# Optimization experiments

Measured on AMD Instinct MI355X. Metric: run time of the kernel, lower is better.

## Reference

```python
import jax, jax.numpy as jnp
import numpy as np

N = 50000   # nodes
C = 128     # channels
H = 2       # heads
E = 800000  # edges (before self loops)


def setup_inputs() -> dict:
    key = jax.random.key(0)
    ks = jax.random.split(key, 8)
    scale = 1.0 / np.sqrt(C)
    x = jax.random.normal(ks[0], (N, C), jnp.float32)
    edge_index = jax.random.randint(ks[1], (2, E), 0, N, jnp.int32)
    W_l = jax.random.normal(ks[2], (H * C, C), jnp.float32) * scale  # lin_l (source/message)
    b_l = jnp.zeros((H * C,), jnp.float32)
    W_r = jax.random.normal(ks[3], (H * C, C), jnp.float32) * scale  # lin_r (target)
    b_r = jnp.zeros((H * C,), jnp.float32)
    att = jax.random.normal(ks[4], (H, C), jnp.float32) * scale      # attention vector per head
    bias = jnp.zeros((C,), jnp.float32)                              # conv output bias (concat=False)
    gn_weight = jnp.ones((C,), jnp.float32)
    gn_bias = jnp.zeros((C,), jnp.float32)
    gn_mean_scale = jnp.ones((C,), jnp.float32)
    return {"x": x, "edge_index": edge_index, "W_l": W_l, "b_l": b_l,
            "W_r": W_r, "b_r": b_r, "att": att, "bias": bias,
            "gn_weight": gn_weight, "gn_bias": gn_bias, "gn_mean_scale": gn_mean_scale}


def reference(x, edge_index, W_l, b_l, W_r, b_r, att, bias, gn_weight, gn_bias, gn_mean_scale):
    n = x.shape[0]
    h, c = att.shape
    # add self loops (PyG default)
    loops = jnp.arange(n, dtype=edge_index.dtype)
    ei = jnp.concatenate([edge_index, jnp.stack([loops, loops])], axis=1)
    src, dst = ei[0], ei[1]
    # GATv2: e_ij = att . leaky_relu(lin_l(x_j) + lin_r(x_i))
    x_l = (x @ W_l.T + b_l).reshape(n, h, c)  # source / message features
    x_r = (x @ W_r.T + b_r).reshape(n, h, c)  # target features
    e = jax.nn.leaky_relu(x_l[src] + x_r[dst], negative_slope=0.2)  # [E', H, C]
    logits = jnp.einsum('ehc,hc->eh', e, att)                        # [E', H]
    # segment softmax over incoming edges of each destination node
    m = jax.ops.segment_max(logits, dst, num_segments=n)             # every node has a self loop
    p = jnp.exp(logits - m[dst])
    s = jax.ops.segment_sum(p, dst, num_segments=n)
    alpha = p / s[dst]                                               # [E', H]
    # weighted scatter-add of messages, then mean over heads (concat=False) + bias
    out = jax.ops.segment_sum(alpha[:, :, None] * x_l[src], dst, num_segments=n)  # [N, H, C]
    out = out.mean(axis=1) + bias                                    # [N, C]
    # GraphNorm (single graph): weight*(x - mean_scale*mean)/sqrt(var+eps) + bias
    mu = out.mean(axis=0)
    o = out - gn_mean_scale * mu
    var = (o * o).mean(axis=0)
    o = gn_weight * o * jax.lax.rsqrt(var + 1e-5) + gn_bias
    o = jax.nn.elu(o)
    return o + x  # residual (shapes match); dropout is identity at eval
```

## Files before the change

kernel.cpp:

```cpp
#include <hip/hip_runtime.h>
#include <stdint.h>

typedef __attribute__((ext_vector_type(8))) short bf16x8;
typedef __attribute__((ext_vector_type(4))) float f32x4;

__device__ inline float u2f(unsigned v){ union{unsigned u; float f;} c; c.u=v; return c.f; }
__device__ inline float f2u_(float){ return 0; }
__device__ inline unsigned short f2bf(float f){
  union{float f; unsigned u;} c; c.f=f;
  unsigned r = c.u + 0x7FFFu + ((c.u>>16)&1u);
  return (unsigned short)(r>>16);
}
__device__ inline unsigned cvtpk_bf16(float lo, float hi){
  unsigned r;
  asm("v_cvt_pk_bf16_f32 %0, %1, %2" : "=v"(r) : "v"(lo), "v"(hi));
  return r;
}
__device__ inline void up8(uint4 u, float4& a0, float4& a1){
  a0.x = u2f(u.x<<16); a0.y = u2f(u.x & 0xFFFF0000u);
  a0.z = u2f(u.y<<16); a0.w = u2f(u.y & 0xFFFF0000u);
  a1.x = u2f(u.z<<16); a1.y = u2f(u.z & 0xFFFF0000u);
  a1.z = u2f(u.w<<16); a1.w = u2f(u.w & 0xFFFF0000u);
}

__global__ void prep_w(const float* __restrict__ Wl, const float* __restrict__ Wr,
                       const float* __restrict__ bl, const float* __restrict__ br,
                       unsigned short* __restrict__ Wb, float* __restrict__ bcat){
  int idx = blockIdx.x*blockDim.x + threadIdx.x;
  if (idx < 512*128){
    int j = idx >> 7, k = idx & 127;
    float v = (j < 256) ? Wl[j*128 + k] : Wr[(j-256)*128 + k];
    Wb[idx] = f2bf(v);
  }
  if (idx < 512) bcat[idx] = (idx < 256) ? bl[idx] : br[idx-256];
}

__launch_bounds__(256)
__global__ void gemm_mfma(const float* __restrict__ x, const unsigned short* __restrict__ Wb,
                          const float* __restrict__ bcat,
                          unsigned short* __restrict__ xl, unsigned short* __restrict__ xr,
                          int n, int* __restrict__ counts, int* __restrict__ total,
                          float* __restrict__ colsum, float* __restrict__ colsq){
  int gid = blockIdx.x*256 + threadIdx.x;
  if (gid < n) counts[gid] = 0;
  if (gid == 0) *total = 0;
  if (gid < 128){ colsum[gid] = 0.f; colsq[gid] = 0.f; }

  int wave = threadIdx.x >> 6, lane = threadIdx.x & 63;
  int lr = lane & 15, kb = (lane >> 4) * 8;
  int rowbase = blockIdx.x*128 + wave*32;

  union FR { bf16x8 v; unsigned u[4]; uint4 u4; };
  FR bfr[2][4];
  int myrow[2]; bool wr[2];
  #pragma unroll
  for (int rg = 0; rg < 2; ++rg){
    myrow[rg] = rowbase + rg*16 + lr;
    int rc = myrow[rg] < n ? myrow[rg] : n-1;
    wr[rg] = myrow[rg] < n;
    const float* xp = &x[(size_t)rc*128];
    #pragma unroll
    for (int ks = 0; ks < 4; ++ks){
      float4 f0 = *reinterpret_cast<const float4*>(xp + ks*32 + kb);
      float4 f1 = *reinterpret_cast<const float4*>(xp + ks*32 + kb + 4);
      bfr[rg][ks].u[0] = cvtpk_bf16(f0.x, f0.y);
      bfr[rg][ks].u[1] = cvtpk_bf16(f0.z, f0.w);
      bfr[rg][ks].u[2] = cvtpk_bf16(f1.x, f1.y);
      bfr[rg][ks].u[3] = cvtpk_bf16(f1.z, f1.w);
    }
  }

  #pragma unroll 1
  for (int mt = 0; mt < 32; ++mt){
    FR afr[4];
    const unsigned short* wp = &Wb[(size_t)(mt*16 + lr)*128 + kb];
    #pragma unroll
    for (int ks = 0; ks < 4; ++ks)
      afr[ks].u4 = *reinterpret_cast<const uint4*>(wp + ks*32);
    f32x4 acc0 = (f32x4){0.f,0.f,0.f,0.f};
    f32x4 acc1 = (f32x4){0.f,0.f,0.f,0.f};
    #pragma unroll
    for (int ks = 0; ks < 4; ++ks){
      acc0 = __builtin_amdgcn_mfma_f32_16x16x32_bf16(afr[ks].v, bfr[0][ks].v, acc0, 0,0,0);
      acc1 = __builtin_amdgcn_mfma_f32_16x16x32_bf16(afr[ks].v, bfr[1][ks].v, acc1, 0,0,0);
    }
    int ch0 = mt*16 + (lane>>4)*4;
    float4 bi = *reinterpret_cast<const float4*>(&bcat[ch0]);
    unsigned short* dst = (ch0 < 256) ? xl : xr;
    int cc = ch0 & 255;
    if (wr[0]){
      uint2 o; o.x = cvtpk_bf16(acc0[0]+bi.x, acc0[1]+bi.y);
      o.y = cvtpk_bf16(acc0[2]+bi.z, acc0[3]+bi.w);
      *reinterpret_cast<uint2*>(&dst[(size_t)myrow[0]*256 + cc]) = o;
    }
    if (wr[1]){
      uint2 o; o.x = cvtpk_bf16(acc1[0]+bi.x, acc1[1]+bi.y);
      o.y = cvtpk_bf16(acc1[2]+bi.z, acc1[3]+bi.w);
      *reinterpret_cast<uint2*>(&dst[(size_t)myrow[1]*256 + cc]) = o;
    }
  }
}

__global__ void hist_dst(const int* __restrict__ ei, int E, int* __restrict__ counts,
                         int* __restrict__ rank){
  for (int e = blockIdx.x*blockDim.x + threadIdx.x; e < E; e += gridDim.x*blockDim.x)
    rank[e] = atomicAdd(&counts[ei[E + e]], 1);
}

__global__ void alloc_offsets(const int* __restrict__ counts, int n, int* __restrict__ offs,
                              int* __restrict__ total){
  int i = blockIdx.x*blockDim.x + threadIdx.x;
  int lane = threadIdx.x & 63;
  int v = (i < n) ? counts[i] : 0;
  int incl = v;
  #pragma unroll
  for (int d = 1; d < 64; d <<= 1){
    int y = __shfl_up(incl, d);
    if (lane >= d) incl += y;
  }
  int wsum = __shfl(incl, 63);
  int base = 0;
  if (lane == 0) base = atomicAdd(total, wsum);
  base = __shfl(base, 0);
  if (i < n) offs[i] = base + incl - v;
}

__global__ void scatter_edges(const int* __restrict__ ei, int E,
                              const int* __restrict__ offs, const int* __restrict__ rank,
                              int* __restrict__ ssrc){
  for (int e = blockIdx.x*blockDim.x + threadIdx.x; e < E; e += gridDim.x*blockDim.x){
    int d = ei[E + e];
    ssrc[offs[d] + rank[e]] = ei[e];
  }
}

__device__ inline float dot8(const float4& a0, const float4& a1,
                             const float4& xr0, const float4& xr1,
                             const float4& at0, const float4& at1){
  float t, d;
  t = a0.x+xr0.x; t = fmaxf(t, 0.2f*t); d  = at0.x*t;
  t = a0.y+xr0.y; t = fmaxf(t, 0.2f*t); d += at0.y*t;
  t = a0.z+xr0.z; t = fmaxf(t, 0.2f*t); d += at0.z*t;
  t = a0.w+xr0.w; t = fmaxf(t, 0.2f*t); d += at0.w*t;
  t = a1.x+xr1.x; t = fmaxf(t, 0.2f*t); d += at1.x*t;
  t = a1.y+xr1.y; t = fmaxf(t, 0.2f*t); d += at1.y*t;
  t = a1.z+xr1.z; t = fmaxf(t, 0.2f*t); d += at1.z*t;
  t = a1.w+xr1.w; t = fmaxf(t, 0.2f*t); d += at1.w*t;
  return d;
}
__device__ inline float red16(float d){
  d += __shfl_xor(d, 1); d += __shfl_xor(d, 2);
  d += __shfl_xor(d, 4); d += __shfl_xor(d, 8);
  return d;
}

__launch_bounds__(128)
__global__ void node_attn(const unsigned short* __restrict__ xl,
                          const unsigned short* __restrict__ xr,
                          const float* __restrict__ att, const float* __restrict__ bias,
                          const int* __restrict__ offs, const int* __restrict__ counts,
                          const int* __restrict__ ssrc,
                          float* __restrict__ out, int n){
  int lane = threadIdx.x & 63;
  int v = blockIdx.x*2 + (threadIdx.x >> 6);
  if (v >= n) return;
  int half = lane >> 5, q5 = lane & 31, h = q5 >> 4, cq = q5 & 15;
  int fbase = h*128 + cq*8;

  float4 xr0, xr1;
  up8(*reinterpret_cast<const uint4*>(&xr[(size_t)v*256 + fbase]), xr0, xr1);
  float4 at0 = *reinterpret_cast<const float4*>(&att[fbase]);
  float4 at1 = *reinterpret_cast<const float4*>(&att[fbase + 4]);

  float4 sv0, sv1;
  up8(*reinterpret_cast<const uint4*>(&xl[(size_t)v*256 + fbase]), sv0, sv1);
  float dself = red16(dot8(sv0, sv1, xr0, xr1, at0, at1));
  float m, s; float4 ac0, ac1;
  if (half == 0){ m = dself; s = 1.f; ac0 = sv0; ac1 = sv1; }
  else { m = -1e30f; s = 0.f; ac0 = make_float4(0,0,0,0); ac1 = ac0; }

  int e0 = offs[v], cnt = counts[v];
  int halfoff = half*4;
  int e = 0;
  while (e < cnt){
    int take = cnt - e; if (take > 64) take = 64;
    int last = e0 + cnt - 1;
    int idx = e0 + e + lane; if (idx > last) idx = last;
    int batch = ssrc[idx];

    uint4 c0, c1, c2, c3;
    {
      int b = halfoff;
      int i0 = __shfl(batch, b),   i1 = __shfl(batch, b+1);
      int i2 = __shfl(batch, b+2), i3 = __shfl(batch, b+3);
      c0 = *reinterpret_cast<const uint4*>(&xl[(size_t)i0*256 + fbase]);
      c1 = *reinterpret_cast<const uint4*>(&xl[(size_t)i1*256 + fbase]);
      c2 = *reinterpret_cast<const uint4*>(&xl[(size_t)i2*256 + fbase]);
      c3 = *reinterpret_cast<const uint4*>(&xl[(size_t)i3*256 + fbase]);
    }
    for (int j = 0; j < take; j += 8){
      uint4 n0, n1, n2, n3;
      bool more = (j + 8) < take;
      if (more){
        int b = j + 8 + halfoff;
        int i0 = __shfl(batch, b),   i1 = __shfl(batch, b+1);
        int i2 = __shfl(batch, b+2), i3 = __shfl(batch, b+3);
        n0 = *reinterpret_cast<const uint4*>(&xl[(size_t)i0*256 + fbase]);
        n1 = *reinterpret_cast<const uint4*>(&xl[(size_t)i1*256 + fbase]);
        n2 = *reinterpret_cast<const uint4*>(&xl[(size_t)i2*256 + fbase]);
        n3 = *reinterpret_cast<const uint4*>(&xl[(size_t)i3*256 + fbase]);
      }
      float4 a00,a01,a10,a11,a20,a21,a30,a31;
      up8(c0, a00, a01); up8(c1, a10, a11);
      up8(c2, a20, a21); up8(c3, a30, a31);
      float d0 = red16(dot8(a00,a01,xr0,xr1,at0,at1));
      float d1 = red16(dot8(a10,a11,xr0,xr1,at0,at1));
      float d2 = red16(dot8(a20,a21,xr0,xr1,at0,at1));
      float d3 = red16(dot8(a30,a31,xr0,xr1,at0,at1));

      float p0e, p1e, p2e, p3e, f;
      if (j + 8 <= take){
        float nm = fmaxf(m, fmaxf(fmaxf(d0,d1), fmaxf(d2,d3)));
        f = __expf(m - nm);
        p0e = __expf(d0-nm); p1e = __expf(d1-nm);
        p2e = __expf(d2-nm); p3e = __expf(d3-nm);
        m = nm;
      } else {
        int b0 = j + halfoff;
        bool v0 = b0 < take, v1 = b0+1 < take, v2 = b0+2 < take, v3 = b0+3 < take;
        float dm0 = v0 ? d0 : -1e30f, dm1 = v1 ? d1 : -1e30f;
        float dm2 = v2 ? d2 : -1e30f, dm3 = v3 ? d3 : -1e30f;
        float nm = fmaxf(m, fmaxf(fmaxf(dm0,dm1), fmaxf(dm2,dm3)));
        f = __expf(m - nm);
        p0e = v0 ? __expf(d0-nm) : 0.f;
        p1e = v1 ? __expf(d1-nm) : 0.f;
        p2e = v2 ? __expf(d2-nm) : 0.f;
        p3e = v3 ? __expf(d3-nm) : 0.f;
        m = nm;
      }
      s = s*f + ((p0e+p1e)+(p2e+p3e));
      ac0.x = ac0.x*f + p0e*a00.x + p1e*a10.x + p2e*a20.x + p3e*a30.x;
      ac0.y = ac0.y*f + p0e*a00.y + p1e*a10.y + p2e*a20.y + p3e*a30.y;
      ac0.z = ac0.z*f + p0e*a00.z + p1e*a10.z + p2e*a20.z + p3e*a30.z;
      ac0.w = ac0.w*f + p0e*a00.w + p1e*a10.w + p2e*a20.w + p3e*a30.w;
      ac1.x = ac1.x*f + p0e*a01.x + p1e*a11.x + p2e*a21.x + p3e*a31.x;
      ac1.y = ac1.y*f + p0e*a01.y + p1e*a11.y + p2e*a21.y + p3e*a31.y;
      ac1.z = ac1.z*f + p0e*a01.z + p1e*a11.z + p2e*a21.z + p3e*a31.z;
      ac1.w = ac1.w*f + p0e*a01.w + p1e*a11.w + p2e*a21.w + p3e*a31.w;
      if (more){ c0 = n0; c1 = n1; c2 = n2; c3 = n3; }
    }
    e += take;
  }

  float mo = __shfl_xor(m, 32), so = __shfl_xor(s, 32);
  float4 bo0, bo1;
  bo0.x = __shfl_xor(ac0.x, 32); bo0.y = __shfl_xor(ac0.y, 32);
  bo0.z = __shfl_xor(ac0.z, 32); bo0.w = __shfl_xor(ac0.w, 32);
  bo1.x = __shfl_xor(ac1.x, 32); bo1.y = __shfl_xor(ac1.y, 32);
  bo1.z = __shfl_xor(ac1.z, 32); bo1.w = __shfl_xor(ac1.w, 32);
  float mm = fmaxf(m, mo);
  float fa = __expf(m - mm), fb = __expf(mo - mm);
  s = s*fa + so*fb;
  ac0.x = ac0.x*fa + bo0.x*fb; ac0.y = ac0.y*fa + bo0.y*fb;
  ac0.z = ac0.z*fa + bo0.z*fb; ac0.w = ac0.w*fa + bo0.w*fb;
  ac1.x = ac1.x*fa + bo1.x*fb; ac1.y = ac1.y*fa + bo1.y*fb;
  ac1.z = ac1.z*fa + bo1.z*fb; ac1.w = ac1.w*fa + bo1.w*fb;
  float inv = 1.f/s;
  float w0x = ac0.x*inv, w0y = ac0.y*inv, w0z = ac0.z*inv, w0w = ac0.w*inv;
  float w1x = ac1.x*inv, w1y = ac1.y*inv, w1z = ac1.z*inv, w1w = ac1.w*inv;
  float o0x = __shfl_xor(w0x, 16), o0y = __shfl_xor(w0y, 16);
  float o0z = __shfl_xor(w0z, 16), o0w = __shfl_xor(w0w, 16);
  float o1x = __shfl_xor(w1x, 16), o1y = __shfl_xor(w1y, 16);
  float o1z = __shfl_xor(w1z, 16), o1w = __shfl_xor(w1w, 16);
  if (half == 0 && h == 0){
    float4 b0 = *reinterpret_cast<const float4*>(&bias[cq*8]);
    float4 b1 = *reinterpret_cast<const float4*>(&bias[cq*8 + 4]);
    float4 r0, r1;
    r0.x = 0.5f*(w0x+o0x) + b0.x; r0.y = 0.5f*(w0y+o0y) + b0.y;
    r0.z = 0.5f*(w0z+o0z) + b0.z; r0.w = 0.5f*(w0w+o0w) + b0.w;
    r1.x = 0.5f*(w1x+o1x) + b1.x; r1.y = 0.5f*(w1y+o1y) + b1.y;
    r1.z = 0.5f*(w1z+o1z) + b1.z; r1.w = 0.5f*(w1w+o1w) + b1.w;
    *reinterpret_cast<float4*>(&out[(size_t)v*128 + cq*8])     = r0;
    *reinterpret_cast<float4*>(&out[(size_t)v*128 + cq*8 + 4]) = r1;
  }
}

__global__ void col_reduce(const float* __restrict__ out, int n,
                           float* __restrict__ colsum, float* __restrict__ colsq){
  __shared__ float s1[256*4], s2[256*4];
  int t = threadIdx.x;
  int c4 = t & 31, rg = t >> 5;
  float4 sum = make_float4(0,0,0,0), sq = make_float4(0,0,0,0);
  for (int r = blockIdx.x*8 + rg; r < n; r += gridDim.x*8){
    float4 v = reinterpret_cast<const float4*>(out)[(size_t)r*32 + c4];
    sum.x += v.x; sum.y += v.y; sum.z += v.z; sum.w += v.w;
    sq.x += v.x*v.x; sq.y += v.y*v.y; sq.z += v.z*v.z; sq.w += v.w*v.w;
  }
  reinterpret_cast<float4*>(s1)[t] = sum;
  reinterpret_cast<float4*>(s2)[t] = sq;
  __syncthreads();
  if (t < 32){
    #pragma unroll
    for (int g = 1; g < 8; ++g){
      float4 a = reinterpret_cast<float4*>(s1)[t + g*32];
      float4 b = reinterpret_cast<float4*>(s2)[t + g*32];
      sum.x += a.x; sum.y += a.y; sum.z += a.z; sum.w += a.w;
      sq.x  += b.x; sq.y  += b.y; sq.z  += b.z; sq.w  += b.w;
    }
    atomicAdd(&colsum[t*4+0], sum.x); atomicAdd(&colsum[t*4+1], sum.y);
    atomicAdd(&colsum[t*4+2], sum.z); atomicAdd(&colsum[t*4+3], sum.w);
    atomicAdd(&colsq[t*4+0], sq.x);  atomicAdd(&colsq[t*4+1], sq.y);
    atomicAdd(&colsq[t*4+2], sq.z);  atomicAdd(&colsq[t*4+3], sq.w);
  }
}

__global__ void fin_stats(const float* __restrict__ colsum, const float* __restrict__ colsq,
                          const float* __restrict__ ms, float* __restrict__ stats, int n){
  int c = threadIdx.x;
  if (c < 128){
    float invn = 1.f/(float)n;
    float mu  = colsum[c]*invn;
    float ex2 = colsq[c]*invn;
    float mm  = ms[c];
    float var = ex2 - 2.f*mm*mu*mu + mm*mm*mu*mu;
    stats[c]     = mm*mu;
    stats[128+c] = rsqrtf(var + 1e-5f);
  }
}

__global__ void final_ew(float* __restrict__ out, const float* __restrict__ x,
                         const float* __restrict__ stats, const float* __restrict__ gw,
                         const float* __restrict__ gb, int n){
  int total = n*32;
  for (int i = blockIdx.x*blockDim.x + threadIdx.x; i < total; i += gridDim.x*blockDim.x){
    int c4 = i & 31;
    float4 o  = reinterpret_cast<float4*>(out)[i];
    float4 xv = reinterpret_cast<const float4*>(x)[i];
    float4 sh = reinterpret_cast<const float4*>(stats)[c4];
    float4 rs = reinterpret_cast<const float4*>(stats)[32 + c4];
    float4 w4 = reinterpret_cast<const float4*>(gw)[c4];
    float4 b4 = reinterpret_cast<const float4*>(gb)[c4];
    float y0 = w4.x*((o.x - sh.x)*rs.x) + b4.x;  y0 = y0 > 0.f ? y0 : expm1f(y0);
    float y1 = w4.y*((o.y - sh.y)*rs.y) + b4.y;  y1 = y1 > 0.f ? y1 : expm1f(y1);
    float y2 = w4.z*((o.z - sh.z)*rs.z) + b4.z;  y2 = y2 > 0.f ? y2 : expm1f(y2);
    float y3 = w4.w*((o.w - sh.w)*rs.w) + b4.w;  y3 = y3 > 0.f ? y3 : expm1f(y3);
    o.x = y0 + xv.x; o.y = y1 + xv.y; o.z = y2 + xv.z; o.w = y3 + xv.w;
    reinterpret_cast<float4*>(out)[i] = o;
  }
}

extern "C" void kernel_launch(void* const* d_in, const int* in_sizes, int n_in,
                              void* d_out, int out_size, void* d_ws, size_t ws_size,
                              hipStream_t stream){
  const float* x    = (const float*)d_in[0];
  const int*   ei   = (const int*)  d_in[1];
  const float* Wl   = (const float*)d_in[2];
  const float* bl   = (const float*)d_in[3];
  const float* Wr   = (const float*)d_in[4];
  const float* br   = (const float*)d_in[5];
  const float* att  = (const float*)d_in[6];
  const float* bias = (const float*)d_in[7];
  const float* gw   = (const float*)d_in[8];
  const float* gb   = (const float*)d_in[9];
  const float* gms  = (const float*)d_in[10];
  int n = in_sizes[0] / 128;
  int E = in_sizes[1] / 2;
  float* outp = (float*)d_out;

  char* w = (char*)d_ws;
  size_t off = 0;
  auto alloc = [&](size_t bytes)->char*{
    char* p = w + off; off += (bytes + 255) & ~(size_t)255; return p;
  };
  unsigned short* xl  = (unsigned short*)alloc((size_t)n*256*2);
  unsigned short* xr  = (unsigned short*)alloc((size_t)n*256*2);
  unsigned short* Wb  = (unsigned short*)alloc(512*128*2);
  float* bcat   = (float*)alloc(512*4);
  int*   counts = (int*)  alloc((size_t)n*4);
  int*   offs   = (int*)  alloc((size_t)n*4);
  int*   total  = (int*)  alloc(4);
  int*   rank   = (int*)  alloc((size_t)E*4);
  int*   ssrc   = (int*)  alloc((size_t)E*4);
  float* colsum = (float*)alloc(128*4);
  float* colsq  = (float*)alloc(128*4);
  float* stats  = (float*)alloc(256*4);
  if (off > ws_size) return;

  prep_w       <<<256, 256, 0, stream>>>(Wl, Wr, bl, br, Wb, bcat);
  gemm_mfma    <<<(n+127)/128, 256, 0, stream>>>(x, Wb, bcat, xl, xr, n, counts, total, colsum, colsq);
  hist_dst     <<<1024, 256, 0, stream>>>(ei, E, counts, rank);
  alloc_offsets<<<(n+255)/256, 256, 0, stream>>>(counts, n, offs, total);
  scatter_edges<<<1024, 256, 0, stream>>>(ei, E, offs, rank, ssrc);
  node_attn    <<<(n+1)/2, 128, 0, stream>>>(xl, xr, att, bias, offs, counts, ssrc, outp, n);
  col_reduce   <<<512, 256, 0, stream>>>(outp, n, colsum, colsq);
  fin_stats    <<<1, 128, 0, stream>>>(colsum, colsq, gms, stats, n);
  final_ew     <<<2048, 256, 0, stream>>>(outp, x, stats, gw, gb, n);
}
```

Baseline: 260.3 us.

## Fuse histogram into GEMM, fold stats into col_reduce, double-prefetch edge gathers

The destination histogram now runs in extra blocks of the GEMM launch, so the two independent jobs overlap in one kernel. Buffer zeroing moves into prep_w. The GraphNorm statistics finalisation moves into col_reduce through a last-block atomic counter, which removes the separate fin_stats launch. In node_attn, the edge loop prefetches two batches of gathered source rows ahead instead of one, hiding more gather latency. The cost is higher register pressure in node_attn and an extra atomic and fence per col_reduce block.

After: 262.5 us. No clear change (+0.9%).

```diff
diff --git a/kernel.cpp b/kernel.cpp
--- a/kernel.cpp
+++ b/kernel.cpp
@@ -5,7 +5,6 @@
 typedef __attribute__((ext_vector_type(4))) float f32x4;
 
 __device__ inline float u2f(unsigned v){ union{unsigned u; float f;} c; c.u=v; return c.f; }
-__device__ inline float f2u_(float){ return 0; }
 __device__ inline unsigned short f2bf(float f){
   union{float f; unsigned u;} c; c.f=f;
   unsigned r = c.u + 0x7FFFu + ((c.u>>16)&1u);
@@ -25,7 +24,10 @@
 
 __global__ void prep_w(const float* __restrict__ Wl, const float* __restrict__ Wr,
                        const float* __restrict__ bl, const float* __restrict__ br,
-                       unsigned short* __restrict__ Wb, float* __restrict__ bcat){
+                       unsigned short* __restrict__ Wb, float* __restrict__ bcat,
+                       int* __restrict__ counts, int* __restrict__ total,
+                       int* __restrict__ done,
+                       float* __restrict__ colsum, float* __restrict__ colsq, int n){
   int idx = blockIdx.x*blockDim.x + threadIdx.x;
   if (idx < 512*128){
     int j = idx >> 7, k = idx & 127;
@@ -33,19 +35,25 @@
     Wb[idx] = f2bf(v);
   }
   if (idx < 512) bcat[idx] = (idx < 256) ? bl[idx] : br[idx-256];
+  if (idx < n) counts[idx] = 0;
+  if (idx < 128){ colsum[idx] = 0.f; colsq[idx] = 0.f; }
+  if (idx == 0){ *total = 0; *done = 0; }
 }
 
 __launch_bounds__(256)
-__global__ void gemm_mfma(const float* __restrict__ x, const unsigned short* __restrict__ Wb,
+__global__ void gemm_hist(const float* __restrict__ x, const unsigned short* __restrict__ Wb,
                           const float* __restrict__ bcat,
                           unsigned short* __restrict__ xl, unsigned short* __restrict__ xr,
-                          int n, int* __restrict__ counts, int* __restrict__ total,
-                          float* __restrict__ colsum, float* __restrict__ colsq){
-  int gid = blockIdx.x*256 + threadIdx.x;
-  if (gid < n) counts[gid] = 0;
-  if (gid == 0) *total = 0;
-  if (gid < 128){ colsum[gid] = 0.f; colsq[gid] = 0.f; }
-
+                          int n, int G,
+                          const int* __restrict__ ei, int E,
+                          int* __restrict__ counts, int* __restrict__ rank){
+  if ((int)blockIdx.x >= G){
+    int hb = blockIdx.x - G;
+    int nb = gridDim.x - G;
+    for (int e = hb*256 + threadIdx.x; e < E; e += nb*256)
+      rank[e] = atomicAdd(&counts[ei[E + e]], 1);
+    return;
+  }
   int wave = threadIdx.x >> 6, lane = threadIdx.x & 63;
   int lr = lane & 15, kb = (lane >> 4) * 8;
   int rowbase = blockIdx.x*128 + wave*32;
@@ -101,12 +109,6 @@
   }
 }
 
-__global__ void hist_dst(const int* __restrict__ ei, int E, int* __restrict__ counts,
-                         int* __restrict__ rank){
-  for (int e = blockIdx.x*blockDim.x + threadIdx.x; e < E; e += gridDim.x*blockDim.x)
-    rank[e] = atomicAdd(&counts[ei[E + e]], 1);
-}
-
 __global__ void alloc_offsets(const int* __restrict__ counts, int n, int* __restrict__ offs,
                               int* __restrict__ total){
   int i = blockIdx.x*blockDim.x + threadIdx.x;
@@ -154,6 +156,59 @@
   return d;
 }
 
+__device__ inline void edge_block(uint4 c0, uint4 c1, uint4 c2, uint4 c3,
+                                  int jb, int halfoff, int take,
+                                  const float4& xr0, const float4& xr1,
+                                  const float4& at0, const float4& at1,
+                                  float& m, float& s, float4& ac0, float4& ac1){
+  float4 a00,a01,a10,a11,a20,a21,a30,a31;
+  up8(c0, a00, a01); up8(c1, a10, a11);
+  up8(c2, a20, a21); up8(c3, a30, a31);
+  float d0 = red16(dot8(a00,a01,xr0,xr1,at0,at1));
+  float d1 = red16(dot8(a10,a11,xr0,xr1,at0,at1));
+  float d2 = red16(dot8(a20,a21,xr0,xr1,at0,at1));
+  float d3 = red16(dot8(a30,a31,xr0,xr1,at0,at1));
+  float p0e, p1e, p2e, p3e, f;
+  if (take - jb >= 8){
+    float nm = fmaxf(m, fmaxf(fmaxf(d0,d1), fmaxf(d2,d3)));
+    f = __expf(m - nm);
+    p0e = __expf(d0-nm); p1e = __expf(d1-nm);
+    p2e = __expf(d2-nm); p3e = __expf(d3-nm);
+    m = nm;
+  } else {
+    int b0 = jb + halfoff;
+    bool v0 = b0 < take, v1 = b0+1 < take, v2 = b0+2 < take, v3 = b0+3 < take;
+    float dm0 = v0 ? d0 : -1e30f, dm1 = v1 ? d1 : -1e30f;
+    float dm2 = v2 ? d2 : -1e30f, dm3 = v3 ? d3 : -1e30f;
+    float nm = fmaxf(m, fmaxf(fmaxf(dm0,dm1), fmaxf(dm2,dm3)));
+    f = __expf(m - nm);
+    p0e = v0 ? __expf(d0-nm) : 0.f;
+    p1e = v1 ? __expf(d1-nm) : 0.f;
+    p2e = v2 ? __expf(d2-nm) : 0.f;
+    p3e = v3 ? __expf(d3-nm) : 0.f;
+    m = nm;
+  }
+  s = s*f + ((p0e+p1e)+(p2e+p3e));
+  ac0.x = ac0.x*f + p0e*a00.x + p1e*a10.x + p2e*a20.x + p3e*a30.x;
+  ac0.y = ac0.y*f + p0e*a00.y + p1e*a10.y + p2e*a20.y + p3e*a30.y;
+  ac0.z = ac0.z*f + p0e*a00.z + p1e*a10.z + p2e*a20.z + p3e*a30.z;
+  ac0.w = ac0.w*f + p0e*a00.w + p1e*a10.w + p2e*a20.w + p3e*a30.w;
+  ac1.x = ac1.x*f + p0e*a01.x + p1e*a11.x + p2e*a21.x + p3e*a31.x;
+  ac1.y = ac1.y*f + p0e*a01.y + p1e*a11.y + p2e*a21.y + p3e*a31.y;
+  ac1.z = ac1.z*f + p0e*a01.z + p1e*a11.z + p2e*a21.z + p3e*a31.z;
+  ac1.w = ac1.w*f + p0e*a01.w + p1e*a11.w + p2e*a21.w + p3e*a31.w;
+}
+
+#define LOADB(X0,X1,X2,X3,JB) do{ \
+  int b_ = (JB) + halfoff; \
+  int i0_ = __shfl(batch, b_),   i1_ = __shfl(batch, b_+1); \
+  int i2_ = __shfl(batch, b_+2), i3_ = __shfl(batch, b_+3); \
+  X0 = *reinterpret_cast<const uint4*>(&xl[(size_t)i0_*256 + fbase]); \
+  X1 = *reinterpret_cast<const uint4*>(&xl[(size_t)i1_*256 + fbase]); \
+  X2 = *reinterpret_cast<const uint4*>(&xl[(size_t)i2_*256 + fbase]); \
+  X3 = *reinterpret_cast<const uint4*>(&xl[(size_t)i3_*256 + fbase]); \
+}while(0)
+
 __launch_bounds__(128)
 __global__ void node_attn(const unsigned short* __restrict__ xl,
                           const unsigned short* __restrict__ xr,
@@ -188,66 +243,19 @@
     int idx = e0 + e + lane; if (idx > last) idx = last;
     int batch = ssrc[idx];
 
-    uint4 c0, c1, c2, c3;
-    {
-      int b = halfoff;
-      int i0 = __shfl(batch, b),   i1 = __shfl(batch, b+1);
-      int i2 = __shfl(batch, b+2), i3 = __shfl(batch, b+3);
-      c0 = *reinterpret_cast<const uint4*>(&xl[(size_t)i0*256 + fbase]);
-      c1 = *reinterpret_cast<const uint4*>(&xl[(size_t)i1*256 + fbase]);
-      c2 = *reinterpret_cast<const uint4*>(&xl[(size_t)i2*256 + fbase]);
-      c3 = *reinterpret_cast<const uint4*>(&xl[(size_t)i3*256 + fbase]);
-    }
-    for (int j = 0; j < take; j += 8){
-      uint4 n0, n1, n2, n3;
-      bool more = (j + 8) < take;
-      if (more){
-        int b = j + 8 + halfoff;
-        int i0 = __shfl(batch, b),   i1 = __shfl(batch, b+1);
-        int i2 = __shfl(batch, b+2), i3 = __shfl(batch, b+3);
-        n0 = *reinterpret_cast<const uint4*>(&xl[(size_t)i0*256 + fbase]);
-        n1 = *reinterpret_cast<const uint4*>(&xl[(size_t)i1*256 + fbase]);
-        n2 = *reinterpret_cast<const uint4*>(&xl[(size_t)i2*256 + fbase]);
-        n3 = *reinterpret_cast<const uint4*>(&xl[(size_t)i3*256 + fbase]);
-      }
-      float4 a00,a01,a10,a11,a20,a21,a30,a31;
-      up8(c0, a00, a01); up8(c1, a10, a11);
-      up8(c2, a20, a21); up8(c3, a30, a31);
-      float d0 = red16(dot8(a00,a01,xr0,xr1,at0,at1));
-      float d1 = red16(dot8(a10,a11,xr0,xr1,at0,at1));
-      float d2 = red16(dot8(a20,a21,xr0,xr1,at0,at1));
-      float d3 = red16(dot8(a30,a31,xr0,xr1,at0,at1));
-
-      float p0e, p1e, p2e, p3e, f;
-      if (j + 8 <= take){
-        float nm = fmaxf(m, fmaxf(fmaxf(d0,d1), fmaxf(d2,d3)));
-        f = __expf(m - nm);
-        p0e = __expf(d0-nm); p1e = __expf(d1-nm);
-        p2e = __expf(d2-nm); p3e = __expf(d3-nm);
-        m = nm;
-      } else {
-        int b0 = j + halfoff;
-        bool v0 = b0 < take, v1 = b0+1 < take, v2 = b0+2 < take, v3 = b0+3 < take;
-        float dm0 = v0 ? d0 : -1e30f, dm1 = v1 ? d1 : -1e30f;
-        float dm2 = v2 ? d2 : -1e30f, dm3 = v3 ? d3 : -1e30f;
-        float nm = fmaxf(m, fmaxf(fmaxf(dm0,dm1), fmaxf(dm2,dm3)));
-        f = __expf(m - nm);
-        p0e = v0 ? __expf(d0-nm) : 0.f;
-        p1e = v1 ? __expf(d1-nm) : 0.f;
-        p2e = v2 ? __expf(d2-nm) : 0.f;
-        p3e = v3 ? __expf(d3-nm) : 0.f;
-        m = nm;
-      }
-      s = s*f + ((p0e+p1e)+(p2e+p3e));
-      ac0.x = ac0.x*f + p0e*a00.x + p1e*a10.x + p2e*a20.x + p3e*a30.x;
-      ac0.y = ac0.y*f + p0e*a00.y + p1e*a10.y + p2e*a20.y + p3e*a30.y;
-      ac0.z = ac0.z*f + p0e*a00.z + p1e*a10.z + p2e*a20.z + p3e*a30.z;
-      ac0.w = ac0.w*f + p0e*a00.w + p1e*a10.w + p2e*a20.w + p3e*a30.w;
-      ac1.x = ac1.x*f + p0e*a01.x + p1e*a11.x + p2e*a21.x + p3e*a31.x;
-      ac1.y = ac1.y*f + p0e*a01.y + p1e*a11.y + p2e*a21.y + p3e*a31.y;
-      ac1.z = ac1.z*f + p0e*a01.z + p1e*a11.z + p2e*a21.z + p3e*a31.z;
-      ac1.w = ac1.w*f + p0e*a01.w + p1e*a11.w + p2e*a21.w + p3e*a31.w;
-      if (more){ c0 = n0; c1 = n1; c2 = n2; c3 = n3; }
+    uint4 A0,A1,A2,A3, B0,B1,B2,B3, P0,P1,P2,P3, Q0,Q1,Q2,Q3;
+    LOADB(A0,A1,A2,A3, 0);
+    if (take > 8) LOADB(B0,B1,B2,B3, 8);
+    else { B0=A0;B1=A1;B2=A2;B3=A3; }
+    P0=A0;P1=A1;P2=A2;P3=A3; Q0=B0;Q1=B1;Q2=B2;Q3=B3;
+
+    for (int j = 0; j < take; j += 16){
+      if (j + 16 < take) LOADB(P0,P1,P2,P3, j+16);
+      edge_block(A0,A1,A2,A3, j, halfoff, take, xr0,xr1,at0,at1, m,s,ac0,ac1);
+      if (j + 24 < take) LOADB(Q0,Q1,Q2,Q3, j+24);
+      if (j + 8 < take)
+        edge_block(B0,B1,B2,B3, j+8, halfoff, take, xr0,xr1,at0,at1, m,s,ac0,ac1);
+      A0=P0;A1=P1;A2=P2;A3=P3; B0=Q0;B1=Q1;B2=Q2;B3=Q3;
     }
     e += take;
   }
@@ -286,8 +294,11 @@
 }
 
 __global__ void col_reduce(const float* __restrict__ out, int n,
-                           float* __restrict__ colsum, float* __restrict__ colsq){
+                           float* __restrict__ colsum, float* __restrict__ colsq,
+                           const float* __restrict__ ms, float* __restrict__ stats,
+                           int* __restrict__ done){
   __shared__ float s1[256*4], s2[256*4];
+  __shared__ int isLast;
   int t = threadIdx.x;
   int c4 = t & 31, rg = t >> 5;
   float4 sum = make_float4(0,0,0,0), sq = make_float4(0,0,0,0);
@@ -312,19 +323,20 @@
     atomicAdd(&colsq[t*4+0], sq.x);  atomicAdd(&colsq[t*4+1], sq.y);
     atomicAdd(&colsq[t*4+2], sq.z);  atomicAdd(&colsq[t*4+3], sq.w);
   }
-}
-
-__global__ void fin_stats(const float* __restrict__ colsum, const float* __restrict__ colsq,
-                          const float* __restrict__ ms, float* __restrict__ stats, int n){
-  int c = threadIdx.x;
-  if (c < 128){
+  __syncthreads();
+  if (t == 0){
+    __threadfence();
+    isLast = (atomicAdd(done, 1) == (int)gridDim.x - 1);
+  }
+  __syncthreads();
+  if (isLast && t < 128){
     float invn = 1.f/(float)n;
-    float mu  = colsum[c]*invn;
-    float ex2 = colsq[c]*invn;
-    float mm  = ms[c];
+    float mu  = colsum[t]*invn;
+    float ex2 = colsq[t]*invn;
+    float mm  = ms[t];
     float var = ex2 - 2.f*mm*mu*mu + mm*mm*mu*mu;
-    stats[c]     = mm*mu;
-    stats[128+c] = rsqrtf(var + 1e-5f);
+    stats[t]     = mm*mu;
+    stats[128+t] = rsqrtf(var + 1e-5f);
   }
 }
 
@@ -379,6 +391,7 @@
   int*   counts = (int*)  alloc((size_t)n*4);
   int*   offs   = (int*)  alloc((size_t)n*4);
   int*   total  = (int*)  alloc(4);
+  int*   done   = (int*)  alloc(4);
   int*   rank   = (int*)  alloc((size_t)E*4);
   int*   ssrc   = (int*)  alloc((size_t)E*4);
   float* colsum = (float*)alloc(128*4);
@@ -386,13 +399,12 @@
   float* stats  = (float*)alloc(256*4);
   if (off > ws_size) return;
 
-  prep_w       <<<256, 256, 0, stream>>>(Wl, Wr, bl, br, Wb, bcat);
-  gemm_mfma    <<<(n+127)/128, 256, 0, stream>>>(x, Wb, bcat, xl, xr, n, counts, total, colsum, colsq);
-  hist_dst     <<<1024, 256, 0, stream>>>(ei, E, counts, rank);
+  int G = (n + 127) / 128;
+  prep_w       <<<256, 256, 0, stream>>>(Wl, Wr, bl, br, Wb, bcat, counts, total, done, colsum, colsq, n);
+  gemm_hist    <<<G + 256, 256, 0, stream>>>(x, Wb, bcat, xl, xr, n, G, ei, E, counts, rank);
   alloc_offsets<<<(n+255)/256, 256, 0, stream>>>(counts, n, offs, total);
   scatter_edges<<<1024, 256, 0, stream>>>(ei, E, offs, rank, ssrc);
   node_attn    <<<(n+1)/2, 128, 0, stream>>>(xl, xr, att, bias, offs, counts, ssrc, outp, n);
-  col_reduce   <<<512, 256, 0, stream>>>(outp, n, colsum, colsq);
-  fin_stats    <<<1, 128, 0, stream>>>(colsum, colsq, gms, stats, n);
+  col_reduce   <<<512, 256, 0, stream>>>(outp, n, colsum, colsq, gms, stats, done);
   final_ew     <<<2048, 256, 0, stream>>>(outp, x, stats, gw, gb, n);
 }
```

## Fuse CSR build into GEMM launch with grid barriers; fold stats into col_reduce

Applied to the files above, without the earlier changes.

The three CSR-building kernels (histogram, offset allocation, scatter) move into 256 extra blocks appended to the GEMM grid. Those blocks synchronise among themselves with atomic spin barriers, so the CSR build can run alongside the projection GEMM instead of after it. The final statistics step is folded into col_reduce using a last-block-done counter, and buffer zeroing moves into prep_w. This cuts launch count and serialization, but relies on all 256 CSR blocks being co-resident to avoid deadlock in the spin barriers.

Result: slower. 351.8 us (+35.1%).

```diff
diff --git a/kernel.cpp b/kernel.cpp
--- a/kernel.cpp
+++ b/kernel.cpp
@@ -5,7 +5,6 @@
 typedef __attribute__((ext_vector_type(4))) float f32x4;
 
 __device__ inline float u2f(unsigned v){ union{unsigned u; float f;} c; c.u=v; return c.f; }
-__device__ inline float f2u_(float){ return 0; }
 __device__ inline unsigned short f2bf(float f){
   union{float f; unsigned u;} c; c.f=f;
   unsigned r = c.u + 0x7FFFu + ((c.u>>16)&1u);
@@ -23,9 +22,22 @@
   a1.z = u2f(u.w<<16); a1.w = u2f(u.w & 0xFFFF0000u);
 }
 
+__device__ inline void gbar(int* ctr, int target){
+  __syncthreads();
+  __threadfence();
+  if (threadIdx.x == 0){
+    atomicAdd(ctr, 1);
+    while (atomicAdd(ctr, 0) < target) __builtin_amdgcn_s_sleep(8);
+  }
+  __syncthreads();
+  __threadfence();
+}
+
 __global__ void prep_w(const float* __restrict__ Wl, const float* __restrict__ Wr,
                        const float* __restrict__ bl, const float* __restrict__ br,
-                       unsigned short* __restrict__ Wb, float* __restrict__ bcat){
+                       unsigned short* __restrict__ Wb, float* __restrict__ bcat,
+                       int* __restrict__ counts, int* __restrict__ zeros4,
+                       float* __restrict__ colsum, float* __restrict__ colsq, int n){
   int idx = blockIdx.x*blockDim.x + threadIdx.x;
   if (idx < 512*128){
     int j = idx >> 7, k = idx & 127;
@@ -33,19 +45,50 @@
     Wb[idx] = f2bf(v);
   }
   if (idx < 512) bcat[idx] = (idx < 256) ? bl[idx] : br[idx-256];
+  if (idx < n) counts[idx] = 0;
+  if (idx < 128){ colsum[idx] = 0.f; colsq[idx] = 0.f; }
+  if (idx < 4) zeros4[idx] = 0;
 }
 
 __launch_bounds__(256)
-__global__ void gemm_mfma(const float* __restrict__ x, const unsigned short* __restrict__ Wb,
-                          const float* __restrict__ bcat,
-                          unsigned short* __restrict__ xl, unsigned short* __restrict__ xr,
-                          int n, int* __restrict__ counts, int* __restrict__ total,
-                          float* __restrict__ colsum, float* __restrict__ colsq){
-  int gid = blockIdx.x*256 + threadIdx.x;
-  if (gid < n) counts[gid] = 0;
-  if (gid == 0) *total = 0;
-  if (gid < 128){ colsum[gid] = 0.f; colsq[gid] = 0.f; }
-
+__global__ void gemm_csr(const float* __restrict__ x, const unsigned short* __restrict__ Wb,
+                         const float* __restrict__ bcat,
+                         unsigned short* __restrict__ xl, unsigned short* __restrict__ xr,
+                         int n, int G,
+                         const int* __restrict__ ei, int E,
+                         int* __restrict__ counts, int* __restrict__ rank,
+                         int* __restrict__ offs, int* __restrict__ ssrc,
+                         int* __restrict__ total, int* __restrict__ bar0,
+                         int* __restrict__ bar1){
+  if ((int)blockIdx.x >= G){
+    const int NB = 256;
+    int cb = blockIdx.x - G;
+    for (int e = cb*256 + threadIdx.x; e < E; e += NB*256)
+      rank[e] = atomicAdd(&counts[ei[E + e]], 1);
+    gbar(bar0, NB);
+    {
+      int i = cb*256 + threadIdx.x;
+      int lane = threadIdx.x & 63;
+      int v = (i < n) ? counts[i] : 0;
+      int incl = v;
+      #pragma unroll
+      for (int d = 1; d < 64; d <<= 1){
+        int y = __shfl_up(incl, d);
+        if (lane >= d) incl += y;
+      }
+      int wsum = __shfl(incl, 63);
+      int base = 0;
+      if (lane == 0) base = atomicAdd(total, wsum);
+      base = __shfl(base, 0);
+      if (i < n) offs[i] = base + incl - v;
+    }
+    gbar(bar1, NB);
+    for (int e = cb*256 + threadIdx.x; e < E; e += NB*256){
+      int d = ei[E + e];
+      ssrc[offs[d] + rank[e]] = ei[e];
+    }
+    return;
+  }
   int wave = threadIdx.x >> 6, lane = threadIdx.x & 63;
   int lr = lane & 15, kb = (lane >> 4) * 8;
   int rowbase = blockIdx.x*128 + wave*32;
@@ -98,39 +141,6 @@
       o.y = cvtpk_bf16(acc1[2]+bi.z, acc1[3]+bi.w);
       *reinterpret_cast<uint2*>(&dst[(size_t)myrow[1]*256 + cc]) = o;
     }
-  }
-}
-
-__global__ void hist_dst(const int* __restrict__ ei, int E, int* __restrict__ counts,
-                         int* __restrict__ rank){
-  for (int e = blockIdx.x*blockDim.x + threadIdx.x; e < E; e += gridDim.x*blockDim.x)
-    rank[e] = atomicAdd(&counts[ei[E + e]], 1);
-}
-
-__global__ void alloc_offsets(const int* __restrict__ counts, int n, int* __restrict__ offs,
-                              int* __restrict__ total){
-  int i = blockIdx.x*blockDim.x + threadIdx.x;
-  int lane = threadIdx.x & 63;
-  int v = (i < n) ? counts[i] : 0;
-  int incl = v;
-  #pragma unroll
-  for (int d = 1; d < 64; d <<= 1){
-    int y = __shfl_up(incl, d);
-    if (lane >= d) incl += y;
-  }
-  int wsum = __shfl(incl, 63);
-  int base = 0;
-  if (lane == 0) base = atomicAdd(total, wsum);
-  base = __shfl(base, 0);
-  if (i < n) offs[i] = base + incl - v;
-}
-
-__global__ void scatter_edges(const int* __restrict__ ei, int E,
-                              const int* __restrict__ offs, const int* __restrict__ rank,
-                              int* __restrict__ ssrc){
-  for (int e = blockIdx.x*blockDim.x + threadIdx.x; e < E; e += gridDim.x*blockDim.x){
-    int d = ei[E + e];
-    ssrc[offs[d] + rank[e]] = ei[e];
   }
 }
 
@@ -286,8 +296,11 @@
 }
 
 __global__ void col_reduce(const float* __restrict__ out, int n,
-                           float* __restrict__ colsum, float* __restrict__ colsq){
+                           float* __restrict__ colsum, float* __restrict__ colsq,
+                           const float* __restrict__ ms, float* __restrict__ stats,
+                           int* __restrict__ done){
   __shared__ float s1[256*4], s2[256*4];
+  __shared__ int isLast;
   int t = threadIdx.x;
   int c4 = t & 31, rg = t >> 5;
   float4 sum = make_float4(0,0,0,0), sq = make_float4(0,0,0,0);
@@ -312,19 +325,20 @@
     atomicAdd(&colsq[t*4+0], sq.x);  atomicAdd(&colsq[t*4+1], sq.y);
     atomicAdd(&colsq[t*4+2], sq.z);  atomicAdd(&colsq[t*4+3], sq.w);
   }
-}
-
-__global__ void fin_stats(const float* __restrict__ colsum, const float* __restrict__ colsq,
-                          const float* __restrict__ ms, float* __restrict__ stats, int n){
-  int c = threadIdx.x;
-  if (c < 128){
+  __syncthreads();
+  if (t == 0){
+    __threadfence();
+    isLast = (atomicAdd(done, 1) == (int)gridDim.x - 1);
+  }
+  __syncthreads();
+  if (isLast && t < 128){
     float invn = 1.f/(float)n;
-    float mu  = colsum[c]*invn;
-    float ex2 = colsq[c]*invn;
-    float mm  = ms[c];
+    float mu  = colsum[t]*invn;
+    float ex2 = colsq[t]*invn;
+    float mm  = ms[t];
     float var = ex2 - 2.f*mm*mu*mu + mm*mm*mu*mu;
-    stats[c]     = mm*mu;
-    stats[128+c] = rsqrtf(var + 1e-5f);
+    stats[t]     = mm*mu;
+    stats[128+t] = rsqrtf(var + 1e-5f);
   }
 }
 
@@ -378,21 +392,23 @@
   float* bcat   = (float*)alloc(512*4);
   int*   counts = (int*)  alloc((size_t)n*4);
   int*   offs   = (int*)  alloc((size_t)n*4);
-  int*   total  = (int*)  alloc(4);
+  int*   zeros4 = (int*)  alloc(4*4);
   int*   rank   = (int*)  alloc((size_t)E*4);
   int*   ssrc   = (int*)  alloc((size_t)E*4);
   float* colsum = (float*)alloc(128*4);
   float* colsq  = (float*)alloc(128*4);
   float* stats  = (float*)alloc(256*4);
   if (off > ws_size) return;
-
-  prep_w       <<<256, 256, 0, stream>>>(Wl, Wr, bl, br, Wb, bcat);
-  gemm_mfma    <<<(n+127)/128, 256, 0, stream>>>(x, Wb, bcat, xl, xr, n, counts, total, colsum, colsq);
-  hist_dst     <<<1024, 256, 0, stream>>>(ei, E, counts, rank);
-  alloc_offsets<<<(n+255)/256, 256, 0, stream>>>(counts, n, offs, total);
-  scatter_edges<<<1024, 256, 0, stream>>>(ei, E, offs, rank, ssrc);
-  node_attn    <<<(n+1)/2, 128, 0, stream>>>(xl, xr, att, bias, offs, counts, ssrc, outp, n);
-  col_reduce   <<<512, 256, 0, stream>>>(outp, n, colsum, colsq);
-  fin_stats    <<<1, 128, 0, stream>>>(colsum, colsq, gms, stats, n);
-  final_ew     <<<2048, 256, 0, stream>>>(outp, x, stats, gw, gb, n);
-}
+  int* total = zeros4 + 0;
+  int* done  = zeros4 + 1;
+  int* bar0  = zeros4 + 2;
+  int* bar1  = zeros4 + 3;
+
+  int G = (n + 127) / 128;
+  prep_w    <<<256, 256, 0, stream>>>(Wl, Wr, bl, br, Wb, bcat, counts, zeros4, colsum, colsq, n);
+  gemm_csr  <<<G + 256, 256, 0, stream>>>(x, Wb, bcat, xl, xr, n, G, ei, E,
+                                          counts, rank, offs, ssrc, total, bar0, bar1);
+  node_attn <<<(n+1)/2, 128, 0, stream>>>(xl, xr, att, bias, offs, counts, ssrc, outp, n);
+  col_reduce<<<512, 256, 0, stream>>>(outp, n, colsum, colsq, gms, stats, done);
+  final_ew  <<<2048, 256, 0, stream>>>(outp, x, stats, gw, gb, n);
+}
```
